# Optimization experiments

Hardware: AMD Instinct MI355X
Metric: run time of the kernel (lower is better)

The kernel has to match this reference:

```python
import jax, jax.numpy as jnp
import numpy as np

U_NODES, V_NODES, N_EDGES = 100000, 50000, 2000000
F_DIM, G_DIM, H_DIM = 32, 32, 8
G_HIDDEN = (64, 32)
F_HIDDEN = (64, 32)
OUT_DIM = 1


def _linear_params(key, din, dout):
    kw, kb = jax.random.split(key)
    lim = 1.0 / np.sqrt(din)
    w = jax.random.uniform(kw, (din, dout), jnp.float32, -lim, lim)
    b = jax.random.uniform(kb, (dout,), jnp.float32, -lim, lim)
    return w, b


def setup_inputs() -> dict:
    key = jax.random.key(0)
    ks = jax.random.split(key, 10)
    u = jax.random.normal(ks[0], (U_NODES, F_DIM), jnp.float32)
    v = jax.random.normal(ks[1], (V_NODES, G_DIM), jnp.float32)
    e_vals = jax.random.normal(ks[2], (N_EDGES, H_DIM), jnp.float32)
    e_src = jax.random.randint(ks[3], (N_EDGES,), 0, V_NODES, jnp.int32)  # V-side index (indices[0])
    e_dst = jax.random.randint(ks[4], (N_EDGES,), 0, U_NODES, jnp.int32)  # U-side index (indices[1])
    g_w1, g_b1 = _linear_params(ks[5], F_DIM + G_DIM + H_DIM, G_HIDDEN[0])
    g_w2, g_b2 = _linear_params(ks[6], G_HIDDEN[0], G_HIDDEN[1])
    f_w1, f_b1 = _linear_params(ks[7], F_DIM + G_HIDDEN[1], F_HIDDEN[0])
    f_w2, f_b2 = _linear_params(ks[8], F_HIDDEN[0], F_HIDDEN[1])
    t_w, t_b = _linear_params(ks[9], F_HIDDEN[1], OUT_DIM)
    return {
        "u": u, "v": v, "e_vals": e_vals, "e_src": e_src, "e_dst": e_dst,
        "g_w1": g_w1, "g_b1": g_b1, "g_w2": g_w2, "g_b2": g_b2,
        "f_w1": f_w1, "f_b1": f_b1, "f_w2": f_w2, "f_b2": f_b2,
        "t_w": t_w, "t_b": t_b,
    }


def reference(u, v, e_vals, e_src, e_dst,
              g_w1, g_b1, g_w2, g_b2,
              f_w1, f_b1, f_w2, f_b2,
              t_w, t_b):
    # gather edge endpoint features -> g MLP (two Linear+ReLU layers)
    edge_in = jnp.concatenate([u[e_dst], v[e_src], e_vals], axis=-1)  # (E, F+G+H)
    h = jax.nn.relu(edge_in @ g_w1 + g_b1)
    h = jax.nn.relu(h @ g_w2 + g_b2)  # (E, D)
    # torch.sparse.sum over dim=-3 (V axis) == segment-sum by the U index
    agg = jax.ops.segment_sum(h, e_dst, num_segments=u.shape[0])  # (U, D)
    # f MLP on concat([u, agg])
    z = jax.nn.relu(jnp.concatenate([u, agg], axis=-1) @ f_w1 + f_b1)
    z = jax.nn.relu(z @ f_w2 + f_b2)
    # tail linear (no relu) + sigmoid
    return jax.nn.sigmoid(z @ t_w + t_b)  # (U, 1)
```

## Files before the change

### kernel.cpp

```cpp
#include <hip/hip_runtime.h>
#include <cstdint>
#include <cstddef>

#define U_NODES 100000
#define V_NODES 50000
#define N_EDGES 2000000


__device__ __forceinline__ void load8f(const float* __restrict__ p, float* x) {
    const float4* p4 = reinterpret_cast<const float4*>(p);
    float4 a = p4[0], b = p4[1];
    x[0]=a.x; x[1]=a.y; x[2]=a.z; x[3]=a.w;
    x[4]=b.x; x[5]=b.y; x[6]=b.z; x[7]=b.w;
}

__device__ __forceinline__ void load32f(const float* __restrict__ p, float* x) {
    #pragma unroll
    for (int q = 0; q < 4; ++q) load8f(p + 8*q, x + 8*q);
}

__device__ __forceinline__ unsigned pack_bf16x2(float a, float b) {
    unsigned ua = __float_as_uint(a);
    ua = (ua + 0x7FFFu + ((ua >> 16) & 1u)) >> 16;
    unsigned ub = __float_as_uint(b);
    ub = (ub + 0x7FFFu + ((ub >> 16) & 1u)) & 0xFFFF0000u;
    return ua | ub;
}


__global__ __launch_bounds__(256) void proj_u_kernel(
    const float* __restrict__ u, const float* __restrict__ g_w1,
    float* __restrict__ A)
{
    int n = blockIdx.x * 256 + threadIdx.x;
    if (n >= U_NODES) return;
    float x[32];
    load32f(u + (size_t)n * 32, x);
    float acc[64];
    #pragma unroll
    for (int j = 0; j < 64; ++j) acc[j] = 0.f;
    #pragma unroll
    for (int i = 0; i < 32; ++i) {
        #pragma unroll
        for (int j = 0; j < 64; ++j) acc[j] += x[i] * g_w1[i*64 + j];
    }
    float4* Ap = reinterpret_cast<float4*>(A + (size_t)n * 64);
    #pragma unroll
    for (int q = 0; q < 16; ++q)
        Ap[q] = make_float4(acc[4*q], acc[4*q+1], acc[4*q+2], acc[4*q+3]);
}

__global__ __launch_bounds__(256) void proj_v_kernel(
    const float* __restrict__ v, const float* __restrict__ g_w1,
    const float* __restrict__ g_b1, float* __restrict__ B)
{
    int n = blockIdx.x * 256 + threadIdx.x;
    if (n >= V_NODES) return;
    float x[32];
    load32f(v + (size_t)n * 32, x);
    float acc[64];
    #pragma unroll
    for (int j = 0; j < 64; ++j) acc[j] = g_b1[j];
    #pragma unroll
    for (int i = 0; i < 32; ++i) {
        #pragma unroll
        for (int j = 0; j < 64; ++j) acc[j] += x[i] * g_w1[(32+i)*64 + j];
    }
    float4* Bp = reinterpret_cast<float4*>(B + (size_t)n * 64);
    #pragma unroll
    for (int q = 0; q < 16; ++q)
        Bp[q] = make_float4(acc[4*q], acc[4*q+1], acc[4*q+2], acc[4*q+3]);
}


__global__ __launch_bounds__(256) void rank_kernel(
    const int* __restrict__ e_dst, int* __restrict__ deg, int* __restrict__ rank)
{
    int e = blockIdx.x * 256 + threadIdx.x;
    if (e >= N_EDGES) return;
    rank[e] = atomicAdd(&deg[e_dst[e]], 1);
}

__global__ __launch_bounds__(256) void scan_block_kernel(
    const int* __restrict__ deg, int* __restrict__ off, int* __restrict__ aux, int n)
{
    __shared__ int s[256];
    int tid = threadIdx.x;
    int i = blockIdx.x * 256 + tid;
    int x = (i < n) ? deg[i] : 0;
    s[tid] = x;
    __syncthreads();
    #pragma unroll
    for (int o = 1; o < 256; o <<= 1) {
        int t = (tid >= o) ? s[tid - o] : 0;
        __syncthreads();
        s[tid] += t;
        __syncthreads();
    }
    if (i < n) off[i + 1] = s[tid];
    if (tid == 255) aux[blockIdx.x] = s[255];
}

__global__ __launch_bounds__(512) void scan_aux_kernel(int* __restrict__ aux, int nA)
{
    __shared__ int s[512];
    int tid = threadIdx.x;
    int x = (tid < nA) ? aux[tid] : 0;
    s[tid] = x;
    __syncthreads();
    #pragma unroll
    for (int o = 1; o < 512; o <<= 1) {
        int t = (tid >= o) ? s[tid - o] : 0;
        __syncthreads();
        s[tid] += t;
        __syncthreads();
    }
    if (tid < nA) aux[tid] = s[tid] - x;
}

__global__ __launch_bounds__(256) void scan_add_kernel(
    int* __restrict__ off, const int* __restrict__ aux, int n)
{
    int i = blockIdx.x * 256 + threadIdx.x;
    if (i == 0) off[0] = 0;
    if (i < n) off[i + 1] += aux[i >> 8];
}

__global__ __launch_bounds__(256) void scatter_kernel(
    const int* __restrict__ e_dst, const int* __restrict__ off,
    const int* __restrict__ rank, int* __restrict__ sorted_eid)
{
    int e = blockIdx.x * 256 + threadIdx.x;
    if (e >= N_EDGES) return;
    int d = e_dst[e];
    sorted_eid[off[d] + rank[e]] = e;
}


template <bool HAS_A, bool HAS_B>
__global__ __launch_bounds__(256) void edge_sorted_kernel(
    const float* __restrict__ A, const float* __restrict__ B,
    const float* __restrict__ u, const float* __restrict__ v,
    const float* __restrict__ e_vals, const int* __restrict__ e_src,
    const int* __restrict__ e_dst, const int* __restrict__ seid,
    const float* __restrict__ g_w1, const float* __restrict__ g_b1,
    const float* __restrict__ g_w2, const float* __restrict__ g_b2,
    float* __restrict__ agg)
{
    __shared__ unsigned lds_h[256][17];
    __shared__ int lds_d[256];
    __shared__ int lds_heads[256];
    __shared__ int lds_cnt;
    __shared__ int lds_prev_d, lds_next_d;

    const int tid = threadIdx.x;
    const long p = (long)blockIdx.x * 256 + tid;

    if (tid == 0) {
        lds_cnt = 0;
        long pprev = (long)blockIdx.x * 256 - 1;
        lds_prev_d = (pprev < 0) ? -2 : e_dst[seid[pprev]];
        long pnext = (long)blockIdx.x * 256 + 256;
        lds_next_d = (pnext >= N_EDGES) ? -2 : e_dst[seid[pnext]];
    }

    int d = -1;
    if (p < N_EDGES) {
        int eid = seid[p];
        d = e_dst[eid];
        int s = e_src[eid];

        float h1[64];
        if constexpr (HAS_A) {
            const float4* Ap = reinterpret_cast<const float4*>(A + (size_t)d * 64);
            #pragma unroll
            for (int q = 0; q < 16; ++q) {
                float4 a = Ap[q];
                h1[4*q+0] = a.x; h1[4*q+1] = a.y; h1[4*q+2] = a.z; h1[4*q+3] = a.w;
            }
        } else {
            #pragma unroll
            for (int j = 0; j < 64; ++j) h1[j] = 0.f;
            float x[32];
            load32f(u + (size_t)d * 32, x);
            #pragma unroll
            for (int i = 0; i < 32; ++i) {
                #pragma unroll
                for (int j = 0; j < 64; ++j) h1[j] += x[i] * g_w1[i*64 + j];
            }
        }
        if constexpr (HAS_B) {
            const float4* Bp = reinterpret_cast<const float4*>(B + (size_t)s * 64);
            #pragma unroll
            for (int q = 0; q < 16; ++q) {
                float4 b = Bp[q];
                h1[4*q+0] += b.x; h1[4*q+1] += b.y; h1[4*q+2] += b.z; h1[4*q+3] += b.w;
            }
        } else {
            #pragma unroll
            for (int j = 0; j < 64; ++j) h1[j] += g_b1[j];
            float x[32];
            load32f(v + (size_t)s * 32, x);
            #pragma unroll
            for (int i = 0; i < 32; ++i) {
                #pragma unroll
                for (int j = 0; j < 64; ++j) h1[j] += x[i] * g_w1[(32+i)*64 + j];
            }
        }
        float ev[8];
        load8f(e_vals + (size_t)eid * 8, ev);
        #pragma unroll
        for (int i = 0; i < 8; ++i) {
            #pragma unroll
            for (int j = 0; j < 64; ++j) h1[j] += ev[i] * g_w1[(64+i)*64 + j];
        }
        #pragma unroll
        for (int j = 0; j < 64; ++j) h1[j] = fmaxf(h1[j], 0.f);

        float h2[32];
        #pragma unroll
        for (int k = 0; k < 32; ++k) h2[k] = g_b2[k];
        #pragma unroll
        for (int i = 0; i < 64; ++i) {
            #pragma unroll
            for (int k = 0; k < 32; ++k) h2[k] += h1[i] * g_w2[i*32 + k];
        }
        #pragma unroll
        for (int cp = 0; cp < 16; ++cp)
            lds_h[tid][cp] = pack_bf16x2(fmaxf(h2[2*cp], 0.f), fmaxf(h2[2*cp+1], 0.f));
    }
    lds_d[tid] = d;
    __syncthreads();

    if (p < N_EDGES) {
        int prevd = (tid == 0) ? lds_prev_d : lds_d[tid - 1];
        bool true_head = (prevd != d);
        bool is_head = (tid == 0) || true_head;
        if (is_head) {
            int idx = atomicAdd(&lds_cnt, 1);
            lds_heads[idx] = tid | (true_head ? 0x10000 : 0);
        }
    }
    __syncthreads();

    const int nseg = lds_cnt;
    const int next_d = lds_next_d;
    for (int w = tid; w < nseg * 16; w += 256) {
        int seg = w >> 4, cp = w & 15;
        int ent = lds_heads[seg];
        int h = ent & 0xFFFF;
        bool thead = (ent & 0x10000) != 0;
        int dd = lds_d[h];
        float s0 = 0.f, s1 = 0.f;
        int r = h;
        while (r < 256 && lds_d[r] == dd) {
            unsigned x = lds_h[r][cp];
            s0 += __uint_as_float(x << 16);
            s1 += __uint_as_float(x & 0xFFFF0000u);
            ++r;
        }
        bool end_complete = (r < 256) || (next_d != dd);
        float* dst = agg + (size_t)dd * 32 + 2 * cp;
        if (thead && end_complete) {
            *reinterpret_cast<float2*>(dst) = make_float2(s0, s1);
        } else {
            atomicAdd(dst + 0, s0);
            atomicAdd(dst + 1, s1);
        }
    }
}


__global__ __launch_bounds__(256) void node_kernel(
    const float* __restrict__ u, const float* __restrict__ agg,
    const float* __restrict__ f_w1, const float* __restrict__ f_b1,
    const float* __restrict__ f_w2, const float* __restrict__ f_b2,
    const float* __restrict__ t_w, const float* __restrict__ t_b,
    float* __restrict__ out)
{
    int n = blockIdx.x * 256 + threadIdx.x;
    if (n >= U_NODES) return;
    float x[64];
    load32f(u   + (size_t)n * 32, x);
    load32f(agg + (size_t)n * 32, x + 32);
    float z1[64];
    #pragma unroll
    for (int j = 0; j < 64; ++j) z1[j] = f_b1[j];
    #pragma unroll
    for (int i = 0; i < 64; ++i) {
        #pragma unroll
        for (int j = 0; j < 64; ++j) z1[j] += x[i] * f_w1[i*64 + j];
    }
    #pragma unroll
    for (int j = 0; j < 64; ++j) z1[j] = fmaxf(z1[j], 0.f);
    float z2[32];
    #pragma unroll
    for (int k = 0; k < 32; ++k) z2[k] = f_b2[k];
    #pragma unroll
    for (int j = 0; j < 64; ++j) {
        #pragma unroll
        for (int k = 0; k < 32; ++k) z2[k] += z1[j] * f_w2[j*32 + k];
    }
    #pragma unroll
    for (int k = 0; k < 32; ++k) z2[k] = fmaxf(z2[k], 0.f);
    float o = t_b[0];
    #pragma unroll
    for (int k = 0; k < 32; ++k) o += z2[k] * t_w[k];
    out[n] = 1.f / (1.f + expf(-o));
}


__global__ __launch_bounds__(256) void edge_direct_kernel(
    const float* __restrict__ u, const float* __restrict__ v,
    const float* __restrict__ e_vals, const int* __restrict__ e_src,
    const int* __restrict__ e_dst, const float* __restrict__ g_w1,
    const float* __restrict__ g_b1, const float* __restrict__ g_w2,
    const float* __restrict__ g_b2, float* __restrict__ agg)
{
    int e = blockIdx.x * 256 + threadIdx.x;
    if (e >= N_EDGES) return;
    int d = e_dst[e];
    int s = e_src[e];
    float x[72];
    load32f(u + (size_t)d * 32, x);
    load32f(v + (size_t)s * 32, x + 32);
    load8f(e_vals + (size_t)e * 8, x + 64);
    float h1[64];
    #pragma unroll
    for (int j = 0; j < 64; ++j) h1[j] = g_b1[j];
    #pragma unroll
    for (int i = 0; i < 72; ++i) {
        #pragma unroll
        for (int j = 0; j < 64; ++j) h1[j] += x[i] * g_w1[i*64 + j];
    }
    #pragma unroll
    for (int j = 0; j < 64; ++j) h1[j] = fmaxf(h1[j], 0.f);
    float acc2[32];
    #pragma unroll
    for (int k = 0; k < 32; ++k) acc2[k] = g_b2[k];
    #pragma unroll
    for (int i = 0; i < 64; ++i) {
        #pragma unroll
        for (int k = 0; k < 32; ++k) acc2[k] += h1[i] * g_w2[i*32 + k];
    }
    float* aggp = agg + (size_t)d * 32;
    #pragma unroll
    for (int k = 0; k < 32; ++k) atomicAdd(aggp + k, fmaxf(acc2[k], 0.f));
}


static inline size_t align256(size_t x) { return (x + 255) & ~(size_t)255; }

extern "C" void kernel_launch(void* const* d_in, const int* in_sizes, int n_in,
                              void* d_out, int out_size, void* d_ws, size_t ws_size,
                              hipStream_t stream) {
    const float* u      = (const float*)d_in[0];
    const float* v      = (const float*)d_in[1];
    const float* e_vals = (const float*)d_in[2];
    const int*   e_src  = (const int*)  d_in[3];
    const int*   e_dst  = (const int*)  d_in[4];
    const float* g_w1   = (const float*)d_in[5];
    const float* g_b1   = (const float*)d_in[6];
    const float* g_w2   = (const float*)d_in[7];
    const float* g_b2   = (const float*)d_in[8];
    const float* f_w1   = (const float*)d_in[9];
    const float* f_b1   = (const float*)d_in[10];
    const float* f_w2   = (const float*)d_in[11];
    const float* f_b2   = (const float*)d_in[12];
    const float* t_w    = (const float*)d_in[13];
    const float* t_b    = (const float*)d_in[14];
    float* out = (float*)d_out;

    char* wsc = (char*)d_ws;
    const int nChunks = (U_NODES + 255) / 256;

    size_t o = 0;
    size_t oDeg  = o; o += align256((size_t)U_NODES * 4);
    size_t oOff  = o; o += align256((size_t)(U_NODES + 1) * 4);
    size_t oAux  = o; o += align256((size_t)nChunks * 4);
    size_t oAgg  = o; o += align256((size_t)U_NODES * 32 * 4);
    size_t oSeid = o; o += align256((size_t)N_EDGES * 4);
    size_t baseNeed = o;
    const size_t rankBytes = align256((size_t)N_EDGES * 4);
    const size_t bBytes    = align256((size_t)V_NODES * 64 * 4);
    const size_t aBytes    = align256((size_t)U_NODES * 64 * 4);

    size_t need1 = baseNeed + bBytes + aBytes;
    size_t need2 = baseNeed + bBytes;
    size_t need3 = baseNeed + rankBytes;

    if (ws_size >= need3) {
        int* deg   = (int*)(wsc + oDeg);
        int* off   = (int*)(wsc + oOff);
        int* aux   = (int*)(wsc + oAux);
        int* seid  = (int*)(wsc + oSeid);
        float* agg = (float*)(wsc + oAgg);

        float* B = nullptr; float* A = nullptr; int* rank;
        bool hasA = false, hasB = false;
        if (ws_size >= need1) {
            B = (float*)(wsc + baseNeed);
            A = (float*)(wsc + baseNeed + bBytes);
            rank = (int*)A;
            hasA = hasB = true;
        } else if (ws_size >= need2) {
            B = (float*)(wsc + baseNeed);
            rank = (int*)B;
            hasB = true;
        } else {
            rank = (int*)(wsc + baseNeed);
        }

        hipMemsetAsync(deg, 0, (size_t)U_NODES * 4, stream);
        hipMemsetAsync(agg, 0, (size_t)U_NODES * 32 * 4, stream);

        rank_kernel<<<(N_EDGES + 255) / 256, 256, 0, stream>>>(e_dst, deg, rank);
        scan_block_kernel<<<nChunks, 256, 0, stream>>>(deg, off, aux, U_NODES);
        scan_aux_kernel<<<1, 512, 0, stream>>>(aux, nChunks);
        scan_add_kernel<<<nChunks, 256, 0, stream>>>(off, aux, U_NODES);
        scatter_kernel<<<(N_EDGES + 255) / 256, 256, 0, stream>>>(e_dst, off, rank, seid);

        if (hasA) {
            proj_v_kernel<<<(V_NODES + 255) / 256, 256, 0, stream>>>(v, g_w1, g_b1, B);
            proj_u_kernel<<<(U_NODES + 255) / 256, 256, 0, stream>>>(u, g_w1, A);
            edge_sorted_kernel<true, true><<<(N_EDGES + 255) / 256, 256, 0, stream>>>(
                A, B, u, v, e_vals, e_src, e_dst, seid, g_w1, g_b1, g_w2, g_b2, agg);
        } else if (hasB) {
            proj_v_kernel<<<(V_NODES + 255) / 256, 256, 0, stream>>>(v, g_w1, g_b1, B);
            edge_sorted_kernel<false, true><<<(N_EDGES + 255) / 256, 256, 0, stream>>>(
                nullptr, B, u, v, e_vals, e_src, e_dst, seid, g_w1, g_b1, g_w2, g_b2, agg);
        } else {
            edge_sorted_kernel<false, false><<<(N_EDGES + 255) / 256, 256, 0, stream>>>(
                nullptr, nullptr, u, v, e_vals, e_src, e_dst, seid, g_w1, g_b1, g_w2, g_b2, agg);
        }
        node_kernel<<<(U_NODES + 255) / 256, 256, 0, stream>>>(
            u, agg, f_w1, f_b1, f_w2, f_b2, t_w, t_b, out);
    } else {
        float* agg = (float*)wsc;
        hipMemsetAsync(agg, 0, (size_t)U_NODES * 32 * 4, stream);
        edge_direct_kernel<<<(N_EDGES + 255) / 256, 256, 0, stream>>>(
            u, v, e_vals, e_src, e_dst, g_w1, g_b1, g_w2, g_b2, agg);
        node_kernel<<<(U_NODES + 255) / 256, 256, 0, stream>>>(
            u, agg, f_w1, f_b1, f_w2, f_b2, t_w, t_b, out);
    }
}
```

Before: 469.3 us.

## Permute edge data into dst-sorted order before the edge MLP kernel

Adds a permute kernel that scatters e_dst, e_src and e_vals into destination-sorted arrays. The edge MLP kernel then reads them contiguously instead of going through an indirection to the sorted edge id. The aim is to replace scattered per-edge reads of e_vals and the index arrays in the hot kernel with coalesced ones. In exchange the scatter pass writes about 40 extra bytes per edge and uses more workspace, with the old path kept as a fallback when workspace is small.

Result: slower. 506.3 us (+7.9%).

```diff
diff --git a/kernel.cpp b/kernel.cpp
--- a/kernel.cpp
+++ b/kernel.cpp
@@ -134,6 +134,147 @@
     if (e >= N_EDGES) return;
     int d = e_dst[e];
     sorted_eid[off[d] + rank[e]] = e;
+}
+
+__global__ __launch_bounds__(256) void permute_kernel(
+    const int* __restrict__ e_dst, const int* __restrict__ e_src,
+    const int* __restrict__ rank, const int* __restrict__ off,
+    const float* __restrict__ e_vals,
+    int* __restrict__ d_sorted, int* __restrict__ s_sorted,
+    float* __restrict__ ev_sorted)
+{
+    int e = blockIdx.x * 256 + threadIdx.x;
+    if (e >= N_EDGES) return;
+    int d = e_dst[e];
+    int pos = off[d] + rank[e];
+    d_sorted[pos] = d;
+    s_sorted[pos] = e_src[e];
+    const float4* src = reinterpret_cast<const float4*>(e_vals + (size_t)e * 8);
+    float4 v0 = src[0], v1 = src[1];
+    float4* dst = reinterpret_cast<float4*>(ev_sorted + (size_t)pos * 8);
+    dst[0] = v0; dst[1] = v1;
+}
+
+
+template <bool HAS_A>
+__global__ __launch_bounds__(256) void edge_perm_kernel(
+    const float* __restrict__ A, const float* __restrict__ B,
+    const float* __restrict__ u,
+    const int* __restrict__ d_sorted, const int* __restrict__ s_sorted,
+    const float* __restrict__ ev_sorted,
+    const float* __restrict__ g_w1, const float* __restrict__ g_w2,
+    const float* __restrict__ g_b2, float* __restrict__ agg)
+{
+    __shared__ unsigned lds_h[256][17];
+    __shared__ int lds_d[256];
+    __shared__ int lds_heads[256];
+    __shared__ int lds_cnt;
+    __shared__ int lds_prev_d, lds_next_d;
+
+    const int tid = threadIdx.x;
+    const long p = (long)blockIdx.x * 256 + tid;
+
+    if (tid == 0) {
+        lds_cnt = 0;
+        long pprev = (long)blockIdx.x * 256 - 1;
+        lds_prev_d = (pprev < 0) ? -2 : d_sorted[pprev];
+        long pnext = (long)blockIdx.x * 256 + 256;
+        lds_next_d = (pnext >= N_EDGES) ? -2 : d_sorted[pnext];
+    }
+
+    int d = -1;
+    if (p < N_EDGES) {
+        d = d_sorted[p];
+        int s = s_sorted[p];
+
+        float h1[64];
+        if constexpr (HAS_A) {
+            const float4* Ap = reinterpret_cast<const float4*>(A + (size_t)d * 64);
+            #pragma unroll
+            for (int q = 0; q < 16; ++q) {
+                float4 a = Ap[q];
+                h1[4*q+0] = a.x; h1[4*q+1] = a.y; h1[4*q+2] = a.z; h1[4*q+3] = a.w;
+            }
+        } else {
+            #pragma unroll
+            for (int j = 0; j < 64; ++j) h1[j] = 0.f;
+            float x[32];
+            load32f(u + (size_t)d * 32, x);
+            #pragma unroll
+            for (int i = 0; i < 32; ++i) {
+                #pragma unroll
+                for (int j = 0; j < 64; ++j) h1[j] += x[i] * g_w1[i*64 + j];
+            }
+        }
+        {
+            const float4* Bp = reinterpret_cast<const float4*>(B + (size_t)s * 64);
+            #pragma unroll
+            for (int q = 0; q < 16; ++q) {
+                float4 b = Bp[q];
+                h1[4*q+0] += b.x; h1[4*q+1] += b.y; h1[4*q+2] += b.z; h1[4*q+3] += b.w;
+            }
+        }
+        float ev[8];
+        load8f(ev_sorted + (size_t)p * 8, ev);
+        #pragma unroll
+        for (int i = 0; i < 8; ++i) {
+            #pragma unroll
+            for (int j = 0; j < 64; ++j) h1[j] += ev[i] * g_w1[(64+i)*64 + j];
+        }
+        #pragma unroll
+        for (int j = 0; j < 64; ++j) h1[j] = fmaxf(h1[j], 0.f);
+
+        float h2[32];
+        #pragma unroll
+        for (int k = 0; k < 32; ++k) h2[k] = g_b2[k];
+        #pragma unroll
+        for (int i = 0; i < 64; ++i) {
+            #pragma unroll
+            for (int k = 0; k < 32; ++k) h2[k] += h1[i] * g_w2[i*32 + k];
+        }
+        #pragma unroll
+        for (int cp = 0; cp < 16; ++cp)
+            lds_h[tid][cp] = pack_bf16x2(fmaxf(h2[2*cp], 0.f), fmaxf(h2[2*cp+1], 0.f));
+    }
+    lds_d[tid] = d;
+    __syncthreads();
+
+    if (p < N_EDGES) {
+        int prevd = (tid == 0) ? lds_prev_d : lds_d[tid - 1];
+        bool true_head = (prevd != d);
+        bool is_head = (tid == 0) || true_head;
+        if (is_head) {
+            int idx = atomicAdd(&lds_cnt, 1);
+            lds_heads[idx] = tid | (true_head ? 0x10000 : 0);
+        }
+    }
+    __syncthreads();
+
+    const int nseg = lds_cnt;
+    const int next_d = lds_next_d;
+    for (int w = tid; w < nseg * 16; w += 256) {
+        int seg = w >> 4, cp = w & 15;
+        int ent = lds_heads[seg];
+        int h = ent & 0xFFFF;
+        bool thead = (ent & 0x10000) != 0;
+        int dd = lds_d[h];
+        float s0 = 0.f, s1 = 0.f;
+        int r = h;
+        while (r < 256 && lds_d[r] == dd) {
+            unsigned x = lds_h[r][cp];
+            s0 += __uint_as_float(x << 16);
+            s1 += __uint_as_float(x & 0xFFFF0000u);
+            ++r;
+        }
+        bool end_complete = (r < 256) || (next_d != dd);
+        float* dst = agg + (size_t)dd * 32 + 2 * cp;
+        if (thead && end_complete) {
+            *reinterpret_cast<float2*>(dst) = make_float2(s0, s1);
+        } else {
+            atomicAdd(dst + 0, s0);
+            atomicAdd(dst + 1, s1);
+        }
+    }
 }
 
 
@@ -373,74 +514,107 @@
 
     char* wsc = (char*)d_ws;
     const int nChunks = (U_NODES + 255) / 256;
+    const int eBlocks = (N_EDGES + 255) / 256;
+
+    const size_t degB  = align256((size_t)U_NODES * 4);
+    const size_t offB  = align256((size_t)(U_NODES + 1) * 4);
+    const size_t auxB  = align256((size_t)nChunks * 4);
+    const size_t aggB  = align256((size_t)U_NODES * 32 * 4);
+    const size_t e4B   = align256((size_t)N_EDGES * 4);
+    const size_t evB   = align256((size_t)N_EDGES * 32);
+    const size_t bB    = align256((size_t)V_NODES * 64 * 4);
+    const size_t aB    = align256((size_t)U_NODES * 64 * 4);
 
     size_t o = 0;
-    size_t oDeg  = o; o += align256((size_t)U_NODES * 4);
-    size_t oOff  = o; o += align256((size_t)(U_NODES + 1) * 4);
-    size_t oAux  = o; o += align256((size_t)nChunks * 4);
-    size_t oAgg  = o; o += align256((size_t)U_NODES * 32 * 4);
-    size_t oSeid = o; o += align256((size_t)N_EDGES * 4);
+    size_t oDeg = o; o += degB;
+    size_t oOff = o; o += offB;
+    size_t oAux = o; o += auxB;
+    size_t oAgg = o; o += aggB;
     size_t baseNeed = o;
-    const size_t rankBytes = align256((size_t)N_EDGES * 4);
-    const size_t bBytes    = align256((size_t)V_NODES * 64 * 4);
-    const size_t aBytes    = align256((size_t)U_NODES * 64 * 4);
-
-    size_t need1 = baseNeed + bBytes + aBytes;
-    size_t need2 = baseNeed + bBytes;
-    size_t need3 = baseNeed + rankBytes;
-
-    if (ws_size >= need3) {
-        int* deg   = (int*)(wsc + oDeg);
-        int* off   = (int*)(wsc + oOff);
-        int* aux   = (int*)(wsc + oAux);
-        int* seid  = (int*)(wsc + oSeid);
-        float* agg = (float*)(wsc + oAgg);
-
-        float* B = nullptr; float* A = nullptr; int* rank;
-        bool hasA = false, hasB = false;
-        if (ws_size >= need1) {
-            B = (float*)(wsc + baseNeed);
-            A = (float*)(wsc + baseNeed + bBytes);
-            rank = (int*)A;
-            hasA = hasB = true;
-        } else if (ws_size >= need2) {
-            B = (float*)(wsc + baseNeed);
-            rank = (int*)B;
-            hasB = true;
-        } else {
-            rank = (int*)(wsc + baseNeed);
-        }
+
+    size_t oDs = o;  o += e4B;
+    size_t oSs = o;  o += e4B;
+    size_t oEv = o;  o += evB;
+    size_t oBn = o;  o += bB;
+    size_t needT2 = o;
+    size_t oAn = o;  o += aB;
+    size_t needT1 = o;
+
+    size_t o3 = baseNeed;
+    size_t oSeid = o3; o3 += e4B;
+    size_t needT4 = o3 + e4B;
+    size_t oB3 = o3;   o3 += bB;
+    size_t oA3 = o3;   o3 += aB;
+    size_t needT3 = o3;
+
+    int* deg   = (int*)(wsc + oDeg);
+    int* off   = (int*)(wsc + oOff);
+    int* aux   = (int*)(wsc + oAux);
+    float* agg = (float*)(wsc + oAgg);
+
+    if (ws_size >= needT2) {
+        const bool hasA = (ws_size >= needT1);
+        int* ds    = (int*)(wsc + oDs);
+        int* ss    = (int*)(wsc + oSs);
+        float* evs = (float*)(wsc + oEv);
+        float* B   = (float*)(wsc + oBn);
+        float* A   = hasA ? (float*)(wsc + oAn) : nullptr;
+        int* rank  = hasA ? (int*)A : (int*)B;
 
         hipMemsetAsync(deg, 0, (size_t)U_NODES * 4, stream);
         hipMemsetAsync(agg, 0, (size_t)U_NODES * 32 * 4, stream);
 
-        rank_kernel<<<(N_EDGES + 255) / 256, 256, 0, stream>>>(e_dst, deg, rank);
+        rank_kernel<<<eBlocks, 256, 0, stream>>>(e_dst, deg, rank);
         scan_block_kernel<<<nChunks, 256, 0, stream>>>(deg, off, aux, U_NODES);
         scan_aux_kernel<<<1, 512, 0, stream>>>(aux, nChunks);
         scan_add_kernel<<<nChunks, 256, 0, stream>>>(off, aux, U_NODES);
-        scatter_kernel<<<(N_EDGES + 255) / 256, 256, 0, stream>>>(e_dst, off, rank, seid);
-
+        permute_kernel<<<eBlocks, 256, 0, stream>>>(e_dst, e_src, rank, off, e_vals,
+                                                    ds, ss, evs);
+        proj_v_kernel<<<(V_NODES + 255) / 256, 256, 0, stream>>>(v, g_w1, g_b1, B);
         if (hasA) {
+            proj_u_kernel<<<(U_NODES + 255) / 256, 256, 0, stream>>>(u, g_w1, A);
+            edge_perm_kernel<true><<<eBlocks, 256, 0, stream>>>(
+                A, B, u, ds, ss, evs, g_w1, g_w2, g_b2, agg);
+        } else {
+            edge_perm_kernel<false><<<eBlocks, 256, 0, stream>>>(
+                nullptr, B, u, ds, ss, evs, g_w1, g_w2, g_b2, agg);
+        }
+        node_kernel<<<(U_NODES + 255) / 256, 256, 0, stream>>>(
+            u, agg, f_w1, f_b1, f_w2, f_b2, t_w, t_b, out);
+    } else if (ws_size >= needT4) {
+        const bool hasAB = (ws_size >= needT3);
+        int* seid = (int*)(wsc + oSeid);
+        float* B = hasAB ? (float*)(wsc + oB3) : nullptr;
+        float* A = hasAB ? (float*)(wsc + oA3) : nullptr;
+        int* rank = hasAB ? (int*)A : (int*)(wsc + oSeid + e4B);
+
+        hipMemsetAsync(deg, 0, (size_t)U_NODES * 4, stream);
+        hipMemsetAsync(agg, 0, (size_t)U_NODES * 32 * 4, stream);
+
+        rank_kernel<<<eBlocks, 256, 0, stream>>>(e_dst, deg, rank);
+        scan_block_kernel<<<nChunks, 256, 0, stream>>>(deg, off, aux, U_NODES);
+        scan_aux_kernel<<<1, 512, 0, stream>>>(aux, nChunks);
+        scan_add_kernel<<<nChunks, 256, 0, stream>>>(off, aux, U_NODES);
+        scatter_kernel<<<eBlocks, 256, 0, stream>>>(e_dst, off, rank, seid);
+
+        if (hasAB) {
             proj_v_kernel<<<(V_NODES + 255) / 256, 256, 0, stream>>>(v, g_w1, g_b1, B);
             proj_u_kernel<<<(U_NODES + 255) / 256, 256, 0, stream>>>(u, g_w1, A);
-            edge_sorted_kernel<true, true><<<(N_EDGES + 255) / 256, 256, 0, stream>>>(
+            edge_sorted_kernel<true, true><<<eBlocks, 256, 0, stream>>>(
                 A, B, u, v, e_vals, e_src, e_dst, seid, g_w1, g_b1, g_w2, g_b2, agg);
-        } else if (hasB) {
-            proj_v_kernel<<<(V_NODES + 255) / 256, 256, 0, stream>>>(v, g_w1, g_b1, B);
-            edge_sorted_kernel<false, true><<<(N_EDGES + 255) / 256, 256, 0, stream>>>(
-                nullptr, B, u, v, e_vals, e_src, e_dst, seid, g_w1, g_b1, g_w2, g_b2, agg);
         } else {
-            edge_sorted_kernel<false, false><<<(N_EDGES + 255) / 256, 256, 0, stream>>>(
-                nullptr, nullptr, u, v, e_vals, e_src, e_dst, seid, g_w1, g_b1, g_w2, g_b2, agg);
+            edge_sorted_kernel<false, false><<<eBlocks, 256, 0, stream>>>(
+                nullptr, nullptr, u, v, e_vals, e_src, e_dst, seid,
+                g_w1, g_b1, g_w2, g_b2, agg);
         }
         node_kernel<<<(U_NODES + 255) / 256, 256, 0, stream>>>(
             u, agg, f_w1, f_b1, f_w2, f_b2, t_w, t_b, out);
     } else {
-        float* agg = (float*)wsc;
-        hipMemsetAsync(agg, 0, (size_t)U_NODES * 32 * 4, stream);
-        edge_direct_kernel<<<(N_EDGES + 255) / 256, 256, 0, stream>>>(
-            u, v, e_vals, e_src, e_dst, g_w1, g_b1, g_w2, g_b2, agg);
+        float* agg0 = (float*)wsc;
+        hipMemsetAsync(agg0, 0, (size_t)U_NODES * 32 * 4, stream);
+        edge_direct_kernel<<<eBlocks, 256, 0, stream>>>(
+            u, v, e_vals, e_src, e_dst, g_w1, g_b1, g_w2, g_b2, agg0);
         node_kernel<<<(U_NODES + 255) / 256, 256, 0, stream>>>(
-            u, agg, f_w1, f_b1, f_w2, f_b2, t_w, t_b, out);
-    }
-}
+            u, agg0, f_w1, f_b1, f_w2, f_b2, t_w, t_b, out);
+    }
+}
```
